# Kernel tuning notes

Hardware: AMD Instinct MI355X
Metric: run time of the kernel (lower is better)

The kernel has to match this reference:

```python
import jax, jax.numpy as jnp
import numpy as np

H = 8          # num_head
HD = 64        # head_dim = hidden_dim // num_head
WIN = 33       # atten_window_size (odd)
MIN_SCORE = -1e9


def setup_inputs() -> dict:
    key = jax.random.key(0)
    ks = jax.random.split(key, 12)
    B, S, D = 8, 4096, 512
    scale = 1.0 / np.sqrt(D).astype(np.float32)

    def lin_w(k):
        return jax.random.normal(k, (D, D), jnp.float32) * scale

    return {
        "query": jax.random.normal(ks[0], (B, S, D), jnp.float32),
        "key": jax.random.normal(ks[1], (B, S, D), jnp.float32),
        "value": jax.random.normal(ks[2], (B, S, D), jnp.float32),
        "mask": jax.random.randint(ks[3], (B, S), 0, 2).astype(bool),
        "Wq": lin_w(ks[4]), "bq": jax.random.normal(ks[5], (D,), jnp.float32) * 0.02,
        "Wk": lin_w(ks[6]), "bk": jax.random.normal(ks[7], (D,), jnp.float32) * 0.02,
        "Wv": lin_w(ks[8]), "bv": jax.random.normal(ks[9], (D,), jnp.float32) * 0.02,
        "Wo": lin_w(ks[10]), "bo": jax.random.normal(ks[11], (D,), jnp.float32) * 0.02,
    }


def reference(query, key, value, mask, Wq, bq, Wk, bk, Wv, bv, Wo, bo):
    B, S, D = query.shape
    half = min(WIN // 2, S // 2)

    def proj_split(x, W, b):
        # nn.Linear: x @ W.T + b; then split heads and flatten (B,H) -> B*H
        y = x @ W.T + b
        return y.reshape(B, S, H, HD).transpose(0, 2, 1, 3).reshape(B * H, S, HD)

    q = proj_split(query, Wq, bq)   # [BH, S, HD]
    k = proj_split(key, Wk, bk)
    v = proj_split(value, Wv, bv)
    # mask expanded over heads; True = masked (LocalAttention semantics)
    m = jnp.broadcast_to(mask[:, None, :], (B, H, S)).reshape(B * H, S)

    # banded scores: one [BH, S] vector per window offset (no sqrt(head_dim) scaling,
    # faithful to LocalAttention)
    scores = []
    for off in range(-half, half + 1):
        if off < 0:
            w = jnp.sum(q[:, -off:] * k[:, :off], axis=-1)
            w = jnp.where(m[:, :off], MIN_SCORE, w)
            w = jnp.pad(w, ((0, 0), (-off, 0)), constant_values=MIN_SCORE)
        elif off == 0:
            w = jnp.where(m, MIN_SCORE, jnp.sum(q * k, axis=-1))
        else:
            w = jnp.sum(q[:, :-off] * k[:, off:], axis=-1)
            w = jnp.where(m[:, off:], MIN_SCORE, w)
            w = jnp.pad(w, ((0, 0), (0, off)), constant_values=MIN_SCORE)
        scores.append(w)
    probs = jax.nn.softmax(jnp.stack(scores, axis=-1), axis=-1)  # [BH, S, 2*half+1]

    # weighted gather of values along the band (dropout=0 -> identity)
    out = jnp.zeros_like(v)
    for i, off in enumerate(range(-half, half + 1)):
        p = probs[:, :, i:i + 1]
        if off < 0:
            out = out + jnp.pad(p[:, -off:] * v[:, :off], ((0, 0), (-off, 0), (0, 0)))
        elif off == 0:
            out = out + p * v
        else:
            out = out + jnp.pad(p[:, :-off] * v[:, off:], ((0, 0), (0, off), (0, 0)))

    out = out.reshape(B, H, S, HD).transpose(0, 2, 1, 3).reshape(B, S, D)
    return out @ Wo.T + bo
```

## Files before the change

### kernel.cpp

```cpp
#include <hip/hip_runtime.h>
#include <hip/hip_bf16.h>
#include <stdint.h>

#define BB 8
#define SS 4096
#define DD 512
#define HH 8
#define HDIM 64

typedef unsigned short u16;
typedef __attribute__((ext_vector_type(4))) float f32x4;
typedef __attribute__((ext_vector_type(4))) short s16x4;
typedef __attribute__((ext_vector_type(8))) short s16x8;
typedef __attribute__((ext_vector_type(4))) unsigned int u32x4;

__device__ __forceinline__ u16 f2bf(float f) {
  uint32_t x = __builtin_bit_cast(uint32_t, f);
  x += 0x7fffu + ((x >> 16) & 1u);
  return (u16)(x >> 16);
}
__device__ __forceinline__ float bf2f(u16 u) {
  uint32_t x = (uint32_t)u << 16;
  return __builtin_bit_cast(float, x);
}

__device__ __forceinline__ void gld_lds16(const void* g, void* l) {
  __builtin_amdgcn_global_load_lds((const __attribute__((address_space(1))) void*)g,
                                   (__attribute__((address_space(3))) void*)l, 16, 0, 0);
}

__global__ void cvt_f32_bf16(const float* __restrict__ in, u16* __restrict__ out, int n8) {
  int i = blockIdx.x * blockDim.x + threadIdx.x;
  const int stride = gridDim.x * blockDim.x;
  for (; i < n8; i += stride) {
    const f32x4 a0 = *(const f32x4*)(in + (size_t)i * 8);
    const f32x4 a1 = *(const f32x4*)(in + (size_t)i * 8 + 4);
    s16x8 pk;
#pragma unroll
    for (int j = 0; j < 4; ++j) pk[j] = (short)f2bf(a0[j]);
#pragma unroll
    for (int j = 0; j < 4; ++j) pk[4 + j] = (short)f2bf(a1[j]);
    *(s16x8*)(out + (size_t)i * 8) = pk;
  }
}

__global__ void cvt_weights(const float* __restrict__ w0, const float* __restrict__ w1,
                            const float* __restrict__ w2, const float* __restrict__ w3,
                            u16* __restrict__ out) {
  int i = blockIdx.x * blockDim.x + threadIdx.x;
  const int n = DD * DD;
  if (i < n) {
    out[i]         = f2bf(w0[i]);
    out[n + i]     = f2bf(w1[i]);
    out[2 * n + i] = f2bf(w2[i]);
    out[3 * n + i] = f2bf(w3[i]);
  }
}

__global__ void mask_unpack(const void* __restrict__ mraw, uint8_t* __restrict__ mk, int n) {
  __shared__ int bad[3];
  __shared__ int mode;
  const int t = threadIdx.x;
  if (t < 3) bad[t] = 0;
  __syncthreads();
  const uint32_t* w = (const uint32_t*)mraw;
  const uint32_t x = w[t];
  const bool w01 = (x == 0u) || (x == 1u);
  const uint32_t ob = x | (x >> 8) | (x >> 16) | (x >> 24);
  const bool u01 = ((ob & 0xFEu) == 0u);
  if (!w01) atomicAdd(&bad[0], 1);
  if (!u01) atomicAdd(&bad[1], 1);
  __syncthreads();
  if (t == 0) mode = (bad[0] == 0) ? 0 : (bad[1] == 0 ? 1 : 2);
  __syncthreads();
  const int md = mode;
  for (int i = blockIdx.x * 256 + t; i < n; i += gridDim.x * 256) {
    uint8_t v;
    if (md == 0)      v = (uint8_t)(w[i] & 1u);
    else if (md == 1) v = ((const uint8_t*)mraw)[i] ? 1 : 0;
    else              v = (w[i] != 0u) ? 1 : 0;
    mk[i] = v;
  }
}

template <typename TC>
__global__ __launch_bounds__(256, 2)
void gemm_db(const u16* __restrict__ A, const u16* __restrict__ Bw,
             const float* __restrict__ bias, TC* __restrict__ C,
             int M, int N, int K) {
  __shared__ __align__(16) u16 sA[2][128 * 64];
  __shared__ __align__(16) u16 sB[2][128 * 64];

  const int tid = threadIdx.x;
  const int lane = tid & 63, wv = tid >> 6;
  const int wr = (wv >> 1) * 64, wc = (wv & 1) * 64;
  const int c = lane & 15, g = lane >> 4;
  const int lid = blockIdx.x;
  const int rb = (lid >> 5) * 8 + (lid & 7);
  const int cb = (lid >> 3) & 3;
  const int col0 = cb * 128, row0 = rb * 128;

  const int srB = tid >> 3, cBc = (tid & 7) ^ ((tid >> 3) & 7);
  const u16* a_src = A + (size_t)(row0 + srB) * K + cBc * 8;
  const u16* b_src = Bw + (size_t)(col0 + srB) * K + cBc * 8;

  auto stage = [&](int buf, int ko) {
#pragma unroll
    for (int i = 0; i < 4; ++i)
      gld_lds16(a_src + (size_t)i * 32 * K + ko, (char*)sA[buf] + i * 4096 + wv * 1024);
#pragma unroll
    for (int i = 0; i < 4; ++i)
      gld_lds16(b_src + (size_t)i * 32 * K + ko, (char*)sB[buf] + i * 4096 + wv * 1024);
  };

  f32x4 acc[4][4];
#pragma unroll
  for (int a = 0; a < 4; ++a)
#pragma unroll
    for (int b = 0; b < 4; ++b) acc[a][b] = (f32x4){0.f, 0.f, 0.f, 0.f};

  const int nkt = K / 64;
  stage(0, 0);
  __syncthreads();
  int cur = 0;
  for (int kt = 0; kt < nkt; ++kt) {
    if (kt + 1 < nkt) stage(cur ^ 1, (kt + 1) * 64);

#pragma unroll
    for (int ks = 0; ks < 2; ++ks) {
      s16x8 af[4], bq[4];
#pragma unroll
      for (int mf = 0; mf < 4; ++mf) {
        const int row = wr + mf * 16 + c;
        af[mf] = *(const s16x8*)&sA[cur][row * 64 + (((ks * 4 + g) ^ (c & 7)) * 8)];
      }
#pragma unroll
      for (int nf = 0; nf < 4; ++nf) {
        const int row = wc + nf * 16 + c;
        bq[nf] = *(const s16x8*)&sB[cur][row * 64 + (((ks * 4 + g) ^ (c & 7)) * 8)];
      }
#pragma unroll
      for (int mf = 0; mf < 4; ++mf)
#pragma unroll
        for (int nf = 0; nf < 4; ++nf)
          acc[mf][nf] = __builtin_amdgcn_mfma_f32_16x16x32_bf16(af[mf], bq[nf], acc[mf][nf], 0, 0, 0);
    }
    __syncthreads();
    cur ^= 1;
  }

#pragma unroll
  for (int nf = 0; nf < 4; ++nf) {
    const int col = col0 + wc + nf * 16 + c;
    const float bv = bias[col];
#pragma unroll
    for (int mf = 0; mf < 4; ++mf) {
#pragma unroll
      for (int i = 0; i < 4; ++i) {
        const int row = row0 + wr + mf * 16 + g * 4 + i;
        const float v = acc[mf][nf][i] + bv;
        if constexpr (sizeof(TC) == 4) C[(size_t)row * N + col] = v;
        else                           C[(size_t)row * N + col] = (TC)f2bf(v);
      }
    }
  }
}

__device__ __forceinline__ void hilo8(const f32x4& a0, const f32x4& a1, s16x8& h, s16x8& l) {
#pragma unroll
  for (int j = 0; j < 4; ++j) {
    const float f = a0[j];
    const u16 hb = f2bf(f);
    h[j] = (short)hb;
    l[j] = (short)f2bf(f - bf2f(hb));
  }
#pragma unroll
  for (int j = 0; j < 4; ++j) {
    const float f = a1[j];
    const u16 hb = f2bf(f);
    h[4 + j] = (short)hb;
    l[4 + j] = (short)f2bf(f - bf2f(hb));
  }
}

#define ACH 4
#define VSTR 100

__global__ __launch_bounds__(256, 4)
void attn_mfma(const float* __restrict__ Qp, const float* __restrict__ Kp,
               const u16* __restrict__ Vp, const uint8_t* __restrict__ mk,
               u16* __restrict__ O) {
  __shared__ u16 sKh[96 * 72];
  __shared__ u16 sKl[96 * 68];
  __shared__ u16 sVT[64 * VSTR];
  __shared__ u16 sM[96];

  const int bh = blockIdx.x;
  const int b = bh >> 3, h = bh & 7;
  const int base0 = blockIdx.y * (64 * ACH);
  const int tid = threadIdx.x;

  const int wv = tid >> 6, lane = tid & 63;
  const int c = lane & 15, g = lane >> 4;
  const int qloc = wv * 16 + c;
  const int kb = wv * 16;

  const int krow0 = tid >> 3, kj = tid & 7;
  const int kks = kj >> 2, kg2 = kj & 3;
  const int vk0 = tid >> 3, vdg8 = tid & 7;

  f32x4 kA0[3], kA1[3];
  s16x8 vR[3];
  u16 mR = 1;
  f32x4 qn0[2], qn1[2];

  auto issue_loads = [&](int cs) {
#pragma unroll
    for (int it = 0; it < 3; ++it) {
      const int row = krow0 + it * 32;
      const int gr = cs - 16 + row;
      if (gr >= 0 && gr < SS) {
        const float* kp = Kp + ((size_t)(b * SS + gr)) * DD + h * HDIM + kks * 32 + kg2 * 4;
        kA0[it] = *(const f32x4*)kp;
        kA1[it] = *(const f32x4*)(kp + 16);
      } else {
        kA0[it] = (f32x4){0.f, 0.f, 0.f, 0.f};
        kA1[it] = (f32x4){0.f, 0.f, 0.f, 0.f};
      }
    }
#pragma unroll
    for (int it = 0; it < 3; ++it) {
      const int k = vk0 + it * 32;
      const int gr = cs - 16 + k;
      if (gr >= 0 && gr < SS)
        vR[it] = *(const s16x8*)(Vp + ((size_t)(b * SS + gr)) * DD + h * HDIM + vdg8 * 8);
      else
        vR[it] = (s16x8){0, 0, 0, 0, 0, 0, 0, 0};
    }
    if (tid < 96) {
      const int gr = cs - 16 + tid;
      mR = (gr < 0 || gr >= SS || mk[b * SS + gr]) ? 1 : 0;
    }
    const float* qp = Qp + ((size_t)(b * SS + cs + qloc)) * DD + h * HDIM;
#pragma unroll
    for (int ks = 0; ks < 2; ++ks) {
      qn0[ks] = *(const f32x4*)(qp + 32 * ks + 4 * g);
      qn1[ks] = *(const f32x4*)(qp + 32 * ks + 16 + 4 * g);
    }
  };

  auto write_stage = [&]() {
#pragma unroll
    for (int it = 0; it < 3; ++it) {
      const int row = krow0 + it * 32;
      s16x8 hh, ll;
      hilo8(kA0[it], kA1[it], hh, ll);
      *(s16x8*)&sKh[row * 72 + kj * 8] = hh;
      *(s16x4*)&sKl[row * 68 + kj * 8]     = (s16x4){ll[0], ll[1], ll[2], ll[3]};
      *(s16x4*)&sKl[row * 68 + kj * 8 + 4] = (s16x4){ll[4], ll[5], ll[6], ll[7]};
    }
#pragma unroll
    for (int it = 0; it < 3; ++it) {
      const int k = vk0 + it * 32;
#pragma unroll
      for (int i = 0; i < 8; ++i)
        sVT[(vdg8 * 8 + i) * VSTR + k] = (u16)vR[it][i];
    }
    if (tid < 96) sM[tid] = mR;
  };

  issue_loads(base0);
  write_stage();
  __syncthreads();

  for (int t = 0; t < ACH; ++t) {
    const int s0 = base0 + t * 64;
    const int qrow = s0 + qloc;

    s16x8 qh[2], qlo[2];
#pragma unroll
    for (int ks = 0; ks < 2; ++ks) hilo8(qn0[ks], qn1[ks], qh[ks], qlo[ks]);

    if (t + 1 < ACH) issue_loads(base0 + (t + 1) * 64);

    f32x4 st[3];
#pragma unroll
    for (int kt = 0; kt < 3; ++kt) st[kt] = (f32x4){0.f, 0.f, 0.f, 0.f};
    __builtin_amdgcn_s_setprio(1);
#pragma unroll
    for (int kt = 0; kt < 3; ++kt) {
      const int krow = kb + kt * 16 + c;
      const int rb72 = krow * 72;
      const int rb68 = krow * 68;
#pragma unroll
      for (int ks = 0; ks < 2; ++ks) {
        const s16x8 kh = *(const s16x8*)&sKh[rb72 + ks * 32 + g * 8];
        const s16x4 l0 = *(const s16x4*)&sKl[rb68 + ks * 32 + g * 8];
        const s16x4 l1 = *(const s16x4*)&sKl[rb68 + ks * 32 + g * 8 + 4];
        const s16x8 kl = (s16x8){l0[0], l0[1], l0[2], l0[3], l1[0], l1[1], l1[2], l1[3]};
        st[kt] = __builtin_amdgcn_mfma_f32_16x16x32_bf16(kh, qh[ks], st[kt], 0, 0, 0);
        st[kt] = __builtin_amdgcn_mfma_f32_16x16x32_bf16(kh, qlo[ks], st[kt], 0, 0, 0);
        st[kt] = __builtin_amdgcn_mfma_f32_16x16x32_bf16(kl, qh[ks], st[kt], 0, 0, 0);
      }
    }
    __builtin_amdgcn_s_setprio(0);

    float mx = -3.0e9f;
#pragma unroll
    for (int kt = 0; kt < 3; ++kt) {
#pragma unroll
      for (int i = 0; i < 4; ++i) {
        const int delta = kt * 16 + 4 * g + i - 16 - c;
        const int key = kb + kt * 16 + 4 * g + i;
        float v;
        if (delta < -16 || delta > 16) v = -2.0e9f;
        else if (sM[key])              v = -1.0e9f;
        else                           v = st[kt][i];
        st[kt][i] = v;
        mx = fmaxf(mx, v);
      }
    }
    mx = fmaxf(mx, __shfl_xor(mx, 16));
    mx = fmaxf(mx, __shfl_xor(mx, 32));
    float sum = 0.f;
#pragma unroll
    for (int kt = 0; kt < 3; ++kt) {
#pragma unroll
      for (int i = 0; i < 4; ++i) {
        const float e = __expf(st[kt][i] - mx);
        st[kt][i] = e;
        sum += e;
      }
    }
    sum += __shfl_xor(sum, 16);
    sum += __shfl_xor(sum, 32);
    const float inv = 1.f / sum;

    s16x8 ph[2];
#pragma unroll
    for (int i = 0; i < 4; ++i) {
      ph[0][i]     = (short)f2bf(st[0][i]);
      ph[0][4 + i] = (short)f2bf(st[1][i]);
      ph[1][i]     = (short)f2bf(st[2][i]);
      ph[1][4 + i] = 0;
    }

    f32x4 ot[4];
#pragma unroll
    for (int dt = 0; dt < 4; ++dt) ot[dt] = (f32x4){0.f, 0.f, 0.f, 0.f};
    __builtin_amdgcn_s_setprio(1);
#pragma unroll
    for (int dt = 0; dt < 4; ++dt) {
      const int rowb = (dt * 16 + c) * VSTR;
      const s16x4 v0 = *(const s16x4*)&sVT[rowb + kb + 4 * g];
      const s16x4 v1 = *(const s16x4*)&sVT[rowb + kb + 16 + 4 * g];
      const s16x8 vh0 = (s16x8){v0[0], v0[1], v0[2], v0[3], v1[0], v1[1], v1[2], v1[3]};
      ot[dt] = __builtin_amdgcn_mfma_f32_16x16x32_bf16(vh0, ph[0], ot[dt], 0, 0, 0);
      const s16x4 v2 = *(const s16x4*)&sVT[rowb + kb + 32 + 4 * g];
      const s16x8 vh1 = (s16x8){v2[0], v2[1], v2[2], v2[3], 0, 0, 0, 0};
      ot[dt] = __builtin_amdgcn_mfma_f32_16x16x32_bf16(vh1, ph[1], ot[dt], 0, 0, 0);
    }
    __builtin_amdgcn_s_setprio(0);

    u16* op = O + ((size_t)(b * SS + qrow)) * DD + h * HDIM;
#pragma unroll
    for (int dt = 0; dt < 4; ++dt) {
      s16x4 pk;
#pragma unroll
      for (int i = 0; i < 4; ++i) pk[i] = (short)f2bf(ot[dt][i] * inv);
      *(s16x4*)&op[dt * 16 + 4 * g] = pk;
    }

    __syncthreads();
    if (t + 1 < ACH) {
      write_stage();
      __syncthreads();
    }
  }
}

__global__ __launch_bounds__(256)
void attn_win(const u16* __restrict__ Qp, const u16* __restrict__ Kp,
              const u16* __restrict__ Vp, const uint8_t* __restrict__ mk,
              u16* __restrict__ O) {
  constexpr int KR = 96;
  __shared__ float sK[KR][HDIM];
  __shared__ float sV[KR][HDIM];
  __shared__ float sMf[KR];

  const int bh = blockIdx.x;
  const int b = bh >> 3, h = bh & 7;
  const int s0 = blockIdx.y * 64;
  const int tid = threadIdx.x;

  for (int c = tid; c < KR * 16; c += 256) {
    const int row = c >> 4, c4 = c & 15;
    const int gr = s0 - 16 + row;
    float kv[4], vv[4];
    if (gr >= 0 && gr < SS) {
      const size_t base = ((size_t)(b * SS + gr)) * DD + h * HDIM + c4 * 4;
      const s16x4 kk = *(const s16x4*)(Kp + base);
      const s16x4 vx = *(const s16x4*)(Vp + base);
#pragma unroll
      for (int i = 0; i < 4; ++i) { kv[i] = bf2f((u16)kk[i]); vv[i] = bf2f((u16)vx[i]); }
    } else {
#pragma unroll
      for (int i = 0; i < 4; ++i) { kv[i] = 0.f; vv[i] = 0.f; }
    }
#pragma unroll
    for (int i = 0; i < 4; ++i) {
      const int d = c4 * 4 + i;
      const int pd = (d & 15) * 4 + (d >> 4);
      sK[row][pd] = kv[i];
      sV[row][pd] = vv[i];
    }
  }
  for (int r = tid; r < KR; r += 256) {
    const int gr = s0 - 16 + r;
    sMf[r] = (gr < 0 || gr >= SS || mk[b * SS + gr]) ? 1.f : 0.f;
  }
  __syncthreads();

  const int wv = tid >> 6, lane = tid & 63;
  const int g = lane >> 4, d16 = lane & 15;

  for (int rr = 0; rr < 16; rr += 4) {
    const int lr = wv * 16 + rr + g;
    const int srow = s0 + lr;
    const u16* qp = Qp + ((size_t)(b * SS + srow)) * DD + h * HDIM;
    float q0 = bf2f(qp[d16]), q1 = bf2f(qp[d16 + 16]), q2 = bf2f(qp[d16 + 32]), q3 = bf2f(qp[d16 + 48]);
    float sc[33];
#pragma unroll
    for (int o = 0; o < 33; ++o) {
      const f32x4 kk = *(const f32x4*)&sK[lr + o][d16 * 4];
      float p = q0 * kk[0] + q1 * kk[1] + q2 * kk[2] + q3 * kk[3];
      p += __shfl_xor(p, 1);
      p += __shfl_xor(p, 2);
      p += __shfl_xor(p, 4);
      p += __shfl_xor(p, 8);
      sc[o] = (sMf[lr + o] != 0.f) ? -1.0e9f : p;
    }
    float mx = sc[0];
#pragma unroll
    for (int o = 1; o < 33; ++o) mx = fmaxf(mx, sc[o]);
    float sum = 0.f;
#pragma unroll
    for (int o = 0; o < 33; ++o) { const float e = __expf(sc[o] - mx); sc[o] = e; sum += e; }
    const float inv = 1.f / sum;
    f32x4 acc = (f32x4){0.f, 0.f, 0.f, 0.f};
#pragma unroll
    for (int o = 0; o < 33; ++o) {
      const f32x4 vx = *(const f32x4*)&sV[lr + o][d16 * 4];
      acc += (sc[o] * inv) * vx;
    }
    u16* op = O + ((size_t)(b * SS + srow)) * DD + h * HDIM;
    op[d16]      = f2bf(acc[0]);
    op[d16 + 16] = f2bf(acc[1]);
    op[d16 + 32] = f2bf(acc[2]);
    op[d16 + 48] = f2bf(acc[3]);
  }
}

extern "C" void kernel_launch(void* const* d_in, const int* in_sizes, int n_in,
                              void* d_out, int out_size, void* d_ws, size_t ws_size,
                              hipStream_t stream) {
  const float* query = (const float*)d_in[0];
  const float* key   = (const float*)d_in[1];
  const float* value = (const float*)d_in[2];
  const void*  mraw  = d_in[3];
  const float* Wq = (const float*)d_in[4];
  const float* bq = (const float*)d_in[5];
  const float* Wk = (const float*)d_in[6];
  const float* bk = (const float*)d_in[7];
  const float* Wv = (const float*)d_in[8];
  const float* bv = (const float*)d_in[9];
  const float* Wo = (const float*)d_in[10];
  const float* bo = (const float*)d_in[11];

  const int M = BB * SS, N = DD, K = DD;

  char* ws = (char*)d_ws;
  size_t off = 0;
  auto carve = [&](size_t bytes) -> char* {
    char* p = ws + off;
    off = (off + bytes + 255) & ~(size_t)255;
    return p;
  };
  u16* wAll   = (u16*)carve((size_t)4 * DD * DD * sizeof(u16));
  uint8_t* mk = (uint8_t*)carve((size_t)BB * SS);
  u16* Xb     = (u16*)carve((size_t)M * DD * 2);

  const size_t qk_f32 = (size_t)M * DD * 4;
  const size_t v_b16  = (size_t)M * DD * 2;
  const bool f32p = (off + 2 * qk_f32 + v_b16 + 1024) <= ws_size;

  cvt_weights<<<(DD * DD + 255) / 256, 256, 0, stream>>>(Wq, Wk, Wv, Wo, wAll);
  mask_unpack<<<16, 256, 0, stream>>>(mraw, mk, BB * SS);

  const int n8 = M * DD / 8;
  const dim3 gc(2048);
  const dim3 gg((M / 128) * (N / 128));
  const dim3 ga(BB * HH, SS / (64 * ACH));
  u16* AO = Xb;

  if (f32p) {
    float* Qf = (float*)carve(qk_f32);
    float* Kf = (float*)carve(qk_f32);
    u16*   Vb = (u16*)carve(v_b16);
    cvt_f32_bf16<<<gc, 256, 0, stream>>>(query, Xb, n8);
    gemm_db<float><<<gg, 256, 0, stream>>>(Xb, wAll,               bq, Qf, M, N, K);
    cvt_f32_bf16<<<gc, 256, 0, stream>>>(key, Xb, n8);
    gemm_db<float><<<gg, 256, 0, stream>>>(Xb, wAll + DD * DD,     bk, Kf, M, N, K);
    cvt_f32_bf16<<<gc, 256, 0, stream>>>(value, Xb, n8);
    gemm_db<u16><<<gg, 256, 0, stream>>>(Xb, wAll + 2 * DD * DD, bv, Vb, M, N, K);
    attn_mfma<<<ga, 256, 0, stream>>>(Qf, Kf, Vb, mk, AO);
    gemm_db<float><<<gg, 256, 0, stream>>>(AO, wAll + 3 * DD * DD, bo, (float*)d_out, M, N, K);
  } else {
    const dim3 ga1(BB * HH, SS / 64);
    u16* Qb = (u16*)carve(v_b16);
    u16* Kb = (u16*)carve(v_b16);
    u16* Vb = (u16*)carve(v_b16);
    cvt_f32_bf16<<<gc, 256, 0, stream>>>(query, Xb, n8);
    gemm_db<u16><<<gg, 256, 0, stream>>>(Xb, wAll,               bq, Qb, M, N, K);
    cvt_f32_bf16<<<gc, 256, 0, stream>>>(key, Xb, n8);
    gemm_db<u16><<<gg, 256, 0, stream>>>(Xb, wAll + DD * DD,     bk, Kb, M, N, K);
    cvt_f32_bf16<<<gc, 256, 0, stream>>>(value, Xb, n8);
    gemm_db<u16><<<gg, 256, 0, stream>>>(Xb, wAll + 2 * DD * DD, bv, Vb, M, N, K);
    attn_win<<<ga1, 256, 0, stream>>>(Qb, Kb, Vb, mk, AO);
    gemm_db<float><<<gg, 256, 0, stream>>>(AO, wAll + 3 * DD * DD, bo, (float*)d_out, M, N, K);
  }
}
```

Baseline: 242.3 us.

## Fuse fp32-to-bf16 input conversion into projection GEMM A-tile loading

```diff
diff --git a/kernel.cpp b/kernel.cpp
--- a/kernel.cpp
+++ b/kernel.cpp
@@ -23,10 +23,24 @@
   uint32_t x = (uint32_t)u << 16;
   return __builtin_bit_cast(float, x);
 }
+__device__ __forceinline__ uint32_t cvtpk(float a, float b) {
+  uint32_t d;
+  asm("v_cvt_pk_bf16_f32 %0, %1, %2" : "=v"(d) : "v"(a), "v"(b));
+  return d;
+}
 
 __device__ __forceinline__ void gld_lds16(const void* g, void* l) {
   __builtin_amdgcn_global_load_lds((const __attribute__((address_space(1))) void*)g,
                                    (__attribute__((address_space(3))) void*)l, 16, 0, 0);
+}
+
+__device__ __forceinline__ s16x4 ld_u16x4(const u16* p) {
+  const uint32_t a = *(const uint32_t*)(p);
+  const uint32_t b = *(const uint32_t*)(p + 2);
+  s16x4 r;
+  r[0] = (short)(a & 0xffff); r[1] = (short)(a >> 16);
+  r[2] = (short)(b & 0xffff); r[3] = (short)(b >> 16);
+  return r;
 }
 
 __global__ void cvt_f32_bf16(const float* __restrict__ in, u16* __restrict__ out, int n8) {
@@ -85,9 +99,9 @@
 
 template <typename TC>
 __global__ __launch_bounds__(256, 2)
-void gemm_db(const u16* __restrict__ A, const u16* __restrict__ Bw,
-             const float* __restrict__ bias, TC* __restrict__ C,
-             int M, int N, int K) {
+void gemm_f32a(const float* __restrict__ A, const u16* __restrict__ Bw,
+               const float* __restrict__ bias, TC* __restrict__ C,
+               int M, int N, int K) {
   __shared__ __align__(16) u16 sA[2][128 * 64];
   __shared__ __align__(16) u16 sB[2][128 * 64];
 
@@ -101,6 +115,111 @@
   const int col0 = cb * 128, row0 = rb * 128;
 
   const int srB = tid >> 3, cBc = (tid & 7) ^ ((tid >> 3) & 7);
+  const u16* b_src = Bw + (size_t)(col0 + srB) * K + cBc * 8;
+  auto stageB = [&](int buf, int ko) {
+#pragma unroll
+    for (int i = 0; i < 4; ++i)
+      gld_lds16(b_src + (size_t)i * 32 * K + ko, (char*)sB[buf] + i * 4096 + wv * 1024);
+  };
+
+  const int art = tid >> 3, ajt = tid & 7;
+  const float* a_src = A + (size_t)(row0 + art) * K + ajt * 8;
+  f32x4 aR[4][2];
+  auto loadA = [&](int ko) {
+#pragma unroll
+    for (int i = 0; i < 4; ++i) {
+      const float* p = a_src + (size_t)(i * 32) * K + ko;
+      aR[i][0] = *(const f32x4*)p;
+      aR[i][1] = *(const f32x4*)(p + 4);
+    }
+  };
+  auto writeA = [&](int buf) {
+#pragma unroll
+    for (int i = 0; i < 4; ++i) {
+      const int row = art + i * 32;
+      const u32x4 dd = (u32x4){cvtpk(aR[i][0][0], aR[i][0][1]), cvtpk(aR[i][0][2], aR[i][0][3]),
+                               cvtpk(aR[i][1][0], aR[i][1][1]), cvtpk(aR[i][1][2], aR[i][1][3])};
+      *(s16x8*)&sA[buf][row * 64 + ((ajt ^ (row & 7)) * 8)] = __builtin_bit_cast(s16x8, dd);
+    }
+  };
+
+  f32x4 acc[4][4];
+#pragma unroll
+  for (int a = 0; a < 4; ++a)
+#pragma unroll
+    for (int b = 0; b < 4; ++b) acc[a][b] = (f32x4){0.f, 0.f, 0.f, 0.f};
+
+  const int nkt = K / 64;
+  loadA(0);
+  stageB(0, 0);
+  writeA(0);
+  __syncthreads();
+  int cur = 0;
+  for (int kt = 0; kt < nkt; ++kt) {
+    if (kt + 1 < nkt) {
+      loadA((kt + 1) * 64);
+      stageB(cur ^ 1, (kt + 1) * 64);
+    }
+
+#pragma unroll
+    for (int ks = 0; ks < 2; ++ks) {
+      s16x8 af[4], bq[4];
+#pragma unroll
+      for (int mf = 0; mf < 4; ++mf) {
+        const int row = wr + mf * 16 + c;
+        af[mf] = *(const s16x8*)&sA[cur][row * 64 + (((ks * 4 + g) ^ (c & 7)) * 8)];
+      }
+#pragma unroll
+      for (int nf = 0; nf < 4; ++nf) {
+        const int row = wc + nf * 16 + c;
+        bq[nf] = *(const s16x8*)&sB[cur][row * 64 + (((ks * 4 + g) ^ (c & 7)) * 8)];
+      }
+#pragma unroll
+      for (int mf = 0; mf < 4; ++mf)
+#pragma unroll
+        for (int nf = 0; nf < 4; ++nf)
+          acc[mf][nf] = __builtin_amdgcn_mfma_f32_16x16x32_bf16(af[mf], bq[nf], acc[mf][nf], 0, 0, 0);
+    }
+    if (kt + 1 < nkt) writeA(cur ^ 1);
+    __syncthreads();
+    cur ^= 1;
+  }
+
+#pragma unroll
+  for (int nf = 0; nf < 4; ++nf) {
+    const int col = col0 + wc + nf * 16 + c;
+    const float bv = bias[col];
+#pragma unroll
+    for (int mf = 0; mf < 4; ++mf) {
+#pragma unroll
+      for (int i = 0; i < 4; ++i) {
+        const int row = row0 + wr + mf * 16 + g * 4 + i;
+        const float v = acc[mf][nf][i] + bv;
+        if constexpr (sizeof(TC) == 4) C[(size_t)row * N + col] = v;
+        else                           C[(size_t)row * N + col] = (TC)f2bf(v);
+      }
+    }
+  }
+}
+
+template <typename TC>
+__global__ __launch_bounds__(256, 2)
+void gemm_db(const u16* __restrict__ A, const u16* __restrict__ Bw,
+             const float* __restrict__ bias, TC* __restrict__ C,
+             int M, int N, int K) {
+  __shared__ __align__(16) u16 sA[2][128 * 64];
+  __shared__ __align__(16) u16 sB[2][128 * 64];
+
+  const int tid = threadIdx.x;
+  const int lane = tid & 63, wv = tid >> 6;
+  const int wr = (wv >> 1) * 64, wc = (wv & 1) * 64;
+  const int c = lane & 15, g = lane >> 4;
+  const int lid = blockIdx.x;
+  const int rb = (lid >> 5) * 8 + (lid & 7);
+  const int cb = (lid >> 3) & 3;
+  const int col0 = cb * 128, row0 = rb * 128;
+
+  const int srB = tid >> 3, cBc = (tid & 7) ^ ((tid >> 3) & 7);
   const u16* a_src = A + (size_t)(row0 + srB) * K + cBc * 8;
   const u16* b_src = Bw + (size_t)(col0 + srB) * K + cBc * 8;
 
@@ -184,7 +303,7 @@
 }
 
 #define ACH 4
-#define VSTR 100
+#define VSTR 98
 
 __global__ __launch_bounds__(256, 4)
 void attn_mfma(const float* __restrict__ Qp, const float* __restrict__ Kp,
@@ -352,11 +471,11 @@
 #pragma unroll
     for (int dt = 0; dt < 4; ++dt) {
       const int rowb = (dt * 16 + c) * VSTR;
-      const s16x4 v0 = *(const s16x4*)&sVT[rowb + kb + 4 * g];
-      const s16x4 v1 = *(const s16x4*)&sVT[rowb + kb + 16 + 4 * g];
+      const s16x4 v0 = ld_u16x4(&sVT[rowb + kb + 4 * g]);
+      const s16x4 v1 = ld_u16x4(&sVT[rowb + kb + 16 + 4 * g]);
       const s16x8 vh0 = (s16x8){v0[0], v0[1], v0[2], v0[3], v1[0], v1[1], v1[2], v1[3]};
       ot[dt] = __builtin_amdgcn_mfma_f32_16x16x32_bf16(vh0, ph[0], ot[dt], 0, 0, 0);
-      const s16x4 v2 = *(const s16x4*)&sVT[rowb + kb + 32 + 4 * g];
+      const s16x4 v2 = ld_u16x4(&sVT[rowb + kb + 32 + 4 * g]);
       const s16x8 vh1 = (s16x8){v2[0], v2[1], v2[2], v2[3], 0, 0, 0, 0};
       ot[dt] = __builtin_amdgcn_mfma_f32_16x16x32_bf16(vh1, ph[1], ot[dt], 0, 0, 0);
     }
@@ -488,38 +607,36 @@
   };
   u16* wAll   = (u16*)carve((size_t)4 * DD * DD * sizeof(u16));
   uint8_t* mk = (uint8_t*)carve((size_t)BB * SS);
-  u16* Xb     = (u16*)carve((size_t)M * DD * 2);
 
   const size_t qk_f32 = (size_t)M * DD * 4;
   const size_t v_b16  = (size_t)M * DD * 2;
-  const bool f32p = (off + 2 * qk_f32 + v_b16 + 1024) <= ws_size;
+  const bool f32p = (off + 2 * qk_f32 + 2 * v_b16 + 1024) <= ws_size;
 
   cvt_weights<<<(DD * DD + 255) / 256, 256, 0, stream>>>(Wq, Wk, Wv, Wo, wAll);
   mask_unpack<<<16, 256, 0, stream>>>(mraw, mk, BB * SS);
 
-  const int n8 = M * DD / 8;
-  const dim3 gc(2048);
   const dim3 gg((M / 128) * (N / 128));
   const dim3 ga(BB * HH, SS / (64 * ACH));
-  u16* AO = Xb;
 
   if (f32p) {
     float* Qf = (float*)carve(qk_f32);
     float* Kf = (float*)carve(qk_f32);
     u16*   Vb = (u16*)carve(v_b16);
-    cvt_f32_bf16<<<gc, 256, 0, stream>>>(query, Xb, n8);
-    gemm_db<float><<<gg, 256, 0, stream>>>(Xb, wAll,               bq, Qf, M, N, K);
-    cvt_f32_bf16<<<gc, 256, 0, stream>>>(key, Xb, n8);
-    gemm_db<float><<<gg, 256, 0, stream>>>(Xb, wAll + DD * DD,     bk, Kf, M, N, K);
-    cvt_f32_bf16<<<gc, 256, 0, stream>>>(value, Xb, n8);
-    gemm_db<u16><<<gg, 256, 0, stream>>>(Xb, wAll + 2 * DD * DD, bv, Vb, M, N, K);
+    u16*   AO = (u16*)carve(v_b16);
+    gemm_f32a<float><<<gg, 256, 0, stream>>>(query, wAll,               bq, Qf, M, N, K);
+    gemm_f32a<float><<<gg, 256, 0, stream>>>(key,   wAll + DD * DD,     bk, Kf, M, N, K);
+    gemm_f32a<u16><<<gg, 256, 0, stream>>>(value, wAll + 2 * DD * DD, bv, Vb, M, N, K);
     attn_mfma<<<ga, 256, 0, stream>>>(Qf, Kf, Vb, mk, AO);
     gemm_db<float><<<gg, 256, 0, stream>>>(AO, wAll + 3 * DD * DD, bo, (float*)d_out, M, N, K);
   } else {
     const dim3 ga1(BB * HH, SS / 64);
+    const int n8 = M * DD / 8;
+    const dim3 gc(2048);
+    u16* Xb = (u16*)carve(v_b16);
     u16* Qb = (u16*)carve(v_b16);
     u16* Kb = (u16*)carve(v_b16);
     u16* Vb = (u16*)carve(v_b16);
+    u16* AO = Xb;
     cvt_f32_bf16<<<gc, 256, 0, stream>>>(query, Xb, n8);
     gemm_db<u16><<<gg, 256, 0, stream>>>(Xb, wAll,               bq, Qb, M, N, K);
     cvt_f32_bf16<<<gc, 256, 0, stream>>>(key, Xb, n8);
```

New measurement: 221.0 us, median of 2. -8.8%, faster.
